# Kernel optimization log

Hardware: AMD Instinct MI355X
Metric: run time of the kernel (lower is better)

The kernel has to match this reference:

```python
import jax, jax.numpy as jnp
import numpy as np

V = 50257       # vocab size (leaves of Huffman tree)
N_DEC = V - 1   # internal decision nodes
D = 1024        # input_size
N_EX = 8192     # number of examples (tokens)
MAX_LEN = 24    # max Huffman path depth


def setup_inputs() -> dict:
    key = jax.random.key(0)
    k_x, k_w, k_t, k_p, k_c, k_l = jax.random.split(key, 6)
    x = jax.random.normal(k_x, (N_EX, D), dtype=jnp.float32)
    W = jax.random.normal(k_w, (N_DEC, D), dtype=jnp.float32) * 0.02
    t = jax.random.randint(k_t, (N_EX,), 0, V, dtype=jnp.int32)
    # padded per-leaf tree paths: decision-node indices and +/-1 branch codes
    paths = jax.random.randint(k_p, (V, MAX_LEN), 0, N_DEC, dtype=jnp.int32)
    codes = jnp.where(jax.random.bernoulli(k_c, 0.5, (V, MAX_LEN)), 1.0, -1.0).astype(jnp.float32)
    lens = jax.random.randint(k_l, (V,), 1, MAX_LEN + 1, dtype=jnp.int32)
    return {"x": x, "W": W, "t": t, "paths": paths, "codes": codes, "lens": lens}


def reference(x, W, t, paths, codes, lens):
    # Per-example tree path: gather the decision nodes / codes for each target leaf.
    node_idx = paths[t]            # [N_EX, MAX_LEN] int32
    code = codes[t]                # [N_EX, MAX_LEN] +/-1
    mask = (jnp.arange(MAX_LEN)[None, :] < lens[t][:, None]).astype(x.dtype)  # [N_EX, MAX_LEN]
    # Irregular gather of W rows along each path, then per-step dot products.
    Wp = W[node_idx]               # [N_EX, MAX_LEN, D]
    wxy = code * jnp.einsum('nd,nld->nl', x, Wp)   # [N_EX, MAX_LEN]
    # Per-decision binary log-loss: log(1 + exp(-wxy)), masked to true path length.
    ls = jax.nn.softplus(-wxy) * mask
    return ls.sum()
```

## Files before the change

kernel.cpp:

```cpp
#include <hip/hip_runtime.h>
#include <math.h>

#define HS_D       1024
#define HS_MAXLEN  24
#define HS_PAIRS   12
#define HS_NBUCKET 512

__global__ __launch_bounds__(256) void hsm_pair_kernel(
    const float* __restrict__ x,
    const float* __restrict__ W,
    const int*   __restrict__ t,
    const int*   __restrict__ paths,
    const float* __restrict__ codes,
    const int*   __restrict__ lens,
    float*       __restrict__ ws,
    int n_ex)
{
    const int tid  = threadIdx.x;
    const int lane = tid & 63;
    const int gw   = blockIdx.x * 4 + (tid >> 6);
    const int n    = gw / HS_PAIRS;
    const int p    = gw % HS_PAIRS;

    const int leaf = t[n];
    const int L    = lens[leaf];
    const int l0   = 2 * p;
    const int l1   = l0 + 1;
    if (l0 >= L) return;

    const int   node0 = paths[leaf * HS_MAXLEN + l0];
    const float c0    = codes[leaf * HS_MAXLEN + l0];
    const bool  v1    = (l1 < L);
    const int   node1 = v1 ? paths[leaf * HS_MAXLEN + l1] : node0;
    const float c1    = v1 ? codes[leaf * HS_MAXLEN + l1] : 1.0f;

    const float4* x4 = (const float4*)(x + (size_t)n     * HS_D);
    const float4* w0 = (const float4*)(W + (size_t)node0 * HS_D);
    const float4* w1 = (const float4*)(W + (size_t)node1 * HS_D);

    float4 xf[4], wf0[4], wf1[4];
#pragma unroll
    for (int j = 0; j < 4; ++j) xf[j]  = x4[j * 64 + lane];
#pragma unroll
    for (int j = 0; j < 4; ++j) wf0[j] = w0[j * 64 + lane];
#pragma unroll
    for (int j = 0; j < 4; ++j) wf1[j] = w1[j * 64 + lane];

    float d0 = 0.0f, d1 = 0.0f;
#pragma unroll
    for (int j = 0; j < 4; ++j) {
        d0 += xf[j].x * wf0[j].x + xf[j].y * wf0[j].y
            + xf[j].z * wf0[j].z + xf[j].w * wf0[j].w;
        d1 += xf[j].x * wf1[j].x + xf[j].y * wf1[j].y
            + xf[j].z * wf1[j].z + xf[j].w * wf1[j].w;
    }

#pragma unroll
    for (int off = 32; off > 0; off >>= 1) {
        d0 += __shfl_down(d0, off);
        d1 += __shfl_down(d1, off);
    }

    if (lane == 0) {
        const float z0 = -c0 * d0;
        float v = fmaxf(z0, 0.0f) + log1pf(expf(-fabsf(z0)));
        if (v1) {
            const float z1 = -c1 * d1;
            v += fmaxf(z1, 0.0f) + log1pf(expf(-fabsf(z1)));
        }
        atomicAdd(&ws[gw & (HS_NBUCKET - 1)], v);
    }
}

__global__ __launch_bounds__(64) void hsm_finish_kernel(
    const float* __restrict__ ws, float* __restrict__ out)
{
    const int lane = threadIdx.x;
    float s = 0.0f;
#pragma unroll
    for (int k = 0; k < HS_NBUCKET / 64; ++k)
        s += ws[lane + 64 * k];
#pragma unroll
    for (int off = 32; off > 0; off >>= 1)
        s += __shfl_down(s, off);
    if (lane == 0) out[0] = s;
}

extern "C" void kernel_launch(void* const* d_in, const int* in_sizes, int n_in,
                              void* d_out, int out_size, void* d_ws, size_t ws_size,
                              hipStream_t stream) {
    const float* x     = (const float*)d_in[0];
    const float* W     = (const float*)d_in[1];
    const int*   t     = (const int*)  d_in[2];
    const int*   paths = (const int*)  d_in[3];
    const float* codes = (const float*)d_in[4];
    const int*   lens  = (const int*)  d_in[5];
    float* out = (float*)d_out;
    float* ws  = (float*)d_ws;

    const int n_ex = in_sizes[2];

    hipMemsetAsync(ws, 0, HS_NBUCKET * sizeof(float), stream);

    const int n_waves  = n_ex * HS_PAIRS;
    const int n_blocks = (n_waves + 3) / 4;
    hsm_pair_kernel<<<n_blocks, 256, 0, stream>>>(x, W, t, paths, codes, lens,
                                                  ws, n_ex);
    hsm_finish_kernel<<<1, 64, 0, stream>>>(ws, out);
}
```

Baseline: 324.6 us.

## Assign one wave per example and loop over path pairs, drop atomics

```diff
diff --git a/kernel.cpp b/kernel.cpp
--- a/kernel.cpp
+++ b/kernel.cpp
@@ -3,10 +3,8 @@
 
 #define HS_D       1024
 #define HS_MAXLEN  24
-#define HS_PAIRS   12
-#define HS_NBUCKET 512
 
-__global__ __launch_bounds__(256) void hsm_pair_kernel(
+__global__ __launch_bounds__(256) void hsm_ex_kernel(
     const float* __restrict__ x,
     const float* __restrict__ W,
     const int*   __restrict__ t,
@@ -18,72 +16,89 @@
 {
     const int tid  = threadIdx.x;
     const int lane = tid & 63;
-    const int gw   = blockIdx.x * 4 + (tid >> 6);
-    const int n    = gw / HS_PAIRS;
-    const int p    = gw % HS_PAIRS;
+    const int n = __builtin_amdgcn_readfirstlane(blockIdx.x * 4 + (tid >> 6));
+    if (n >= n_ex) return;
 
-    const int leaf = t[n];
-    const int L    = lens[leaf];
-    const int l0   = 2 * p;
-    const int l1   = l0 + 1;
-    if (l0 >= L) return;
+    const int leaf = __builtin_amdgcn_readfirstlane(t[n]);
+    const int L    = __builtin_amdgcn_readfirstlane(lens[leaf]);
 
-    const int   node0 = paths[leaf * HS_MAXLEN + l0];
-    const float c0    = codes[leaf * HS_MAXLEN + l0];
-    const bool  v1    = (l1 < L);
-    const int   node1 = v1 ? paths[leaf * HS_MAXLEN + l1] : node0;
-    const float c1    = v1 ? codes[leaf * HS_MAXLEN + l1] : 1.0f;
+    const float4* x4 = (const float4*)(x + (size_t)n * HS_D);
+    float4 xf[4];
+#pragma unroll
+    for (int j = 0; j < 4; ++j) xf[j] = x4[j * 64 + lane];
 
-    const float4* x4 = (const float4*)(x + (size_t)n     * HS_D);
-    const float4* w0 = (const float4*)(W + (size_t)node0 * HS_D);
-    const float4* w1 = (const float4*)(W + (size_t)node1 * HS_D);
+    const int*   prow = paths + leaf * HS_MAXLEN;
+    const float* crow = codes + leaf * HS_MAXLEN;
 
-    float4 xf[4], wf0[4], wf1[4];
+    float vsum = 0.0f;
+
+    for (int l0 = 0; l0 < L; l0 += 2) {
+        const int  l1 = l0 + 1;
+        const bool v1 = (l1 < L);
+
+        const int   node0 = __builtin_amdgcn_readfirstlane(prow[l0]);
+        const float c0    = crow[l0];
+        const int   node1 = __builtin_amdgcn_readfirstlane(v1 ? prow[l1] : node0);
+        const float c1    = v1 ? crow[l1] : 1.0f;
+
+        const float4* w0 = (const float4*)(W + (size_t)node0 * HS_D);
+        const float4* w1 = (const float4*)(W + (size_t)node1 * HS_D);
+
+        float4 wf0[4], wf1[4];
 #pragma unroll
-    for (int j = 0; j < 4; ++j) xf[j]  = x4[j * 64 + lane];
+        for (int j = 0; j < 4; ++j) wf0[j] = w0[j * 64 + lane];
 #pragma unroll
-    for (int j = 0; j < 4; ++j) wf0[j] = w0[j * 64 + lane];
+        for (int j = 0; j < 4; ++j) wf1[j] = w1[j * 64 + lane];
+
+        float d0 = 0.0f, d1 = 0.0f;
 #pragma unroll
-    for (int j = 0; j < 4; ++j) wf1[j] = w1[j * 64 + lane];
-
-    float d0 = 0.0f, d1 = 0.0f;
-#pragma unroll
-    for (int j = 0; j < 4; ++j) {
-        d0 += xf[j].x * wf0[j].x + xf[j].y * wf0[j].y
-            + xf[j].z * wf0[j].z + xf[j].w * wf0[j].w;
-        d1 += xf[j].x * wf1[j].x + xf[j].y * wf1[j].y
-            + xf[j].z * wf1[j].z + xf[j].w * wf1[j].w;
-    }
+        for (int j = 0; j < 4; ++j) {
+            d0 += xf[j].x * wf0[j].x + xf[j].y * wf0[j].y
+                + xf[j].z * wf0[j].z + xf[j].w * wf0[j].w;
+            d1 += xf[j].x * wf1[j].x + xf[j].y * wf1[j].y
+                + xf[j].z * wf1[j].z + xf[j].w * wf1[j].w;
+        }
 
 #pragma unroll
-    for (int off = 32; off > 0; off >>= 1) {
-        d0 += __shfl_down(d0, off);
-        d1 += __shfl_down(d1, off);
-    }
+        for (int off = 32; off > 0; off >>= 1) {
+            d0 += __shfl_xor(d0, off);
+            d1 += __shfl_xor(d1, off);
+        }
 
-    if (lane == 0) {
         const float z0 = -c0 * d0;
         float v = fmaxf(z0, 0.0f) + log1pf(expf(-fabsf(z0)));
         if (v1) {
             const float z1 = -c1 * d1;
             v += fmaxf(z1, 0.0f) + log1pf(expf(-fabsf(z1)));
         }
-        atomicAdd(&ws[gw & (HS_NBUCKET - 1)], v);
+        vsum += v;
     }
+
+    if (lane == 0) ws[n] = vsum;
 }
 
-__global__ __launch_bounds__(64) void hsm_finish_kernel(
-    const float* __restrict__ ws, float* __restrict__ out)
+__global__ __launch_bounds__(256) void hsm_finish_kernel(
+    const float* __restrict__ ws, float* __restrict__ out, int n_ex)
 {
-    const int lane = threadIdx.x;
+    __shared__ float part[4];
+    const int tid = threadIdx.x;
+
     float s = 0.0f;
-#pragma unroll
-    for (int k = 0; k < HS_NBUCKET / 64; ++k)
-        s += ws[lane + 64 * k];
+    const int n4 = n_ex >> 2;
+    const float4* w4 = (const float4*)ws;
+    for (int k = tid; k < n4; k += 256) {
+        const float4 v = w4[k];
+        s += v.x + v.y + v.z + v.w;
+    }
+    if (tid < (n_ex & 3)) s += ws[(n_ex & ~3) + tid];
+
 #pragma unroll
     for (int off = 32; off > 0; off >>= 1)
-        s += __shfl_down(s, off);
-    if (lane == 0) out[0] = s;
+        s += __shfl_xor(s, off);
+
+    if ((tid & 63) == 0) part[tid >> 6] = s;
+    __syncthreads();
+    if (tid == 0) out[0] = part[0] + part[1] + part[2] + part[3];
 }
 
 extern "C" void kernel_launch(void* const* d_in, const int* in_sizes, int n_in,
@@ -100,11 +115,8 @@
 
     const int n_ex = in_sizes[2];
 
-    hipMemsetAsync(ws, 0, HS_NBUCKET * sizeof(float), stream);
-
-    const int n_waves  = n_ex * HS_PAIRS;
-    const int n_blocks = (n_waves + 3) / 4;
-    hsm_pair_kernel<<<n_blocks, 256, 0, stream>>>(x, W, t, paths, codes, lens,
-                                                  ws, n_ex);
-    hsm_finish_kernel<<<1, 64, 0, stream>>>(ws, out);
+    const int n_blocks = (n_ex + 3) / 4;
+    hsm_ex_kernel<<<n_blocks, 256, 0, stream>>>(x, W, t, paths, codes, lens,
+                                                ws, n_ex);
+    hsm_finish_kernel<<<1, 256, 0, stream>>>(ws, out, n_ex);
 }
```

After: 335.0 us. 3.2% more time.
